# Performance work log

Measured on AMD Instinct MI355X. Metric: run time of the kernel, lower is better.

Reference implementation:

```python
import jax, jax.numpy as jnp
import numpy as np

C = 6.5  # ALCOVE specificity constant

BATCH, NE, NDIMS = 2048, 2048, 128


def setup_inputs() -> dict:
    key = jax.random.key(0)
    k1, k2, k3 = jax.random.split(key, 3)
    inputs = jax.random.normal(k1, (BATCH, NDIMS), dtype=jnp.float32)
    exemplars = jax.random.normal(k2, (NE, NDIMS), dtype=jnp.float32)
    # attn initialized to ones/ndims in the original; use positive random values
    # scaled similarly so the exp argument stays in a reasonable range.
    attn = jax.random.uniform(k3, (NDIMS,), dtype=jnp.float32) / float(NDIMS)
    return {"inputs": inputs, "exemplars": exemplars, "attn": attn}


def reference(inputs, exemplars, attn):
    # Vectorized form of: exp(-c * sum_d attn_d * |exemplars - x|) per example.
    # diff: (batch, ne, ndims)
    diff = jnp.abs(exemplars[None, :, :] - inputs[:, None, :])
    dist = jnp.einsum('bed,d->be', diff, attn)  # weighted L1 distance
    return jnp.exp(-C * dist)  # (batch, ne)
```

## Files before the change

kernel.cpp:

```cpp
#include <hip/hip_runtime.h>
#include <stdint.h>


#define BATCH 2048
#define NE 2048
#define ND 128

#define TB 64
#define TE 64
#define KC 64

#define QSCALE 16777216.0f
#define QBIAS  2097152.5f
#define KEXP   (-6.5f / 16777216.0f)

#define SAD(acc, a, b) asm("v_sad_u32 %0, %1, %2, %0" : "+v"(acc) : "v"(a), "v"(b))

__global__ __launch_bounds__(256, 4)
void alcove_rbf_kernel(const float* __restrict__ X,
                       const float* __restrict__ E,
                       const float* __restrict__ A,
                       float* __restrict__ out) {
  __shared__ uint32_t Xs[KC * TB];
  __shared__ uint32_t Es[KC * TE];

  const int tid = threadIdx.x;
  const int e0 = blockIdx.x * TE;
  const int b0 = blockIdx.y * TB;

  const int tx = tid & 15;
  const int ty = tid >> 4;
  const int lane_in = tid & 3;

  uint32_t acc[4][4];
#pragma unroll
  for (int j = 0; j < 4; ++j)
#pragma unroll
    for (int i = 0; i < 4; ++i) acc[j][i] = 0u;

  for (int kc = 0; kc < ND; kc += KC) {
    if (kc) __syncthreads();

    const float4* A4 = reinterpret_cast<const float4*>(A + kc);

#pragma unroll
    for (int it = 0; it < 4; ++it) {
      int g = it * 64 + (tid >> 2);
      int row = g & (TB - 1);
      int c4 = 4 * (g >> 6) + lane_in;
      float4 a = A4[c4];
      float4 as;
      as.x = a.x * QSCALE; as.y = a.y * QSCALE;
      as.z = a.z * QSCALE; as.w = a.w * QSCALE;
      int dbase = 4 * c4;

      float4 vx = reinterpret_cast<const float4*>(X + (size_t)(b0 + row) * ND + kc)[c4];
      Xs[(dbase + 0) * TB + row] = (uint32_t)fmaf(vx.x, as.x, QBIAS);
      Xs[(dbase + 1) * TB + row] = (uint32_t)fmaf(vx.y, as.y, QBIAS);
      Xs[(dbase + 2) * TB + row] = (uint32_t)fmaf(vx.z, as.z, QBIAS);
      Xs[(dbase + 3) * TB + row] = (uint32_t)fmaf(vx.w, as.w, QBIAS);

      float4 ve = reinterpret_cast<const float4*>(E + (size_t)(e0 + row) * ND + kc)[c4];
      Es[(dbase + 0) * TE + row] = (uint32_t)fmaf(ve.x, as.x, QBIAS);
      Es[(dbase + 1) * TE + row] = (uint32_t)fmaf(ve.y, as.y, QBIAS);
      Es[(dbase + 2) * TE + row] = (uint32_t)fmaf(ve.z, as.z, QBIAS);
      Es[(dbase + 3) * TE + row] = (uint32_t)fmaf(ve.w, as.w, QBIAS);
    }
    __syncthreads();

    const uint4* Xs4 = reinterpret_cast<const uint4*>(Xs);
    const uint4* Es4 = reinterpret_cast<const uint4*>(Es);
#pragma unroll 4
    for (int d = 0; d < KC; ++d) {
      uint4 xv = Xs4[d * (TB / 4) + ty];
      uint4 ev = Es4[d * (TE / 4) + tx];
      SAD(acc[0][0], xv.x, ev.x); SAD(acc[0][1], xv.x, ev.y);
      SAD(acc[0][2], xv.x, ev.z); SAD(acc[0][3], xv.x, ev.w);
      SAD(acc[1][0], xv.y, ev.x); SAD(acc[1][1], xv.y, ev.y);
      SAD(acc[1][2], xv.y, ev.z); SAD(acc[1][3], xv.y, ev.w);
      SAD(acc[2][0], xv.z, ev.x); SAD(acc[2][1], xv.z, ev.y);
      SAD(acc[2][2], xv.z, ev.z); SAD(acc[2][3], xv.z, ev.w);
      SAD(acc[3][0], xv.w, ev.x); SAD(acc[3][1], xv.w, ev.y);
      SAD(acc[3][2], xv.w, ev.z); SAD(acc[3][3], xv.w, ev.w);
    }
  }

#pragma unroll
  for (int j = 0; j < 4; ++j) {
    int b = b0 + 4 * ty + j;
    float4 o;
    o.x = __expf(KEXP * (float)acc[j][0]);
    o.y = __expf(KEXP * (float)acc[j][1]);
    o.z = __expf(KEXP * (float)acc[j][2]);
    o.w = __expf(KEXP * (float)acc[j][3]);
    reinterpret_cast<float4*>(out + (size_t)b * NE + e0)[tx] = o;
  }
}

extern "C" void kernel_launch(void* const* d_in, const int* in_sizes, int n_in,
                              void* d_out, int out_size, void* d_ws, size_t ws_size,
                              hipStream_t stream) {
  const float* X = (const float*)d_in[0];
  const float* E = (const float*)d_in[1];
  const float* A = (const float*)d_in[2];
  float* out = (float*)d_out;

  dim3 grid(NE / TE, BATCH / TB);
  dim3 block(256);
  alcove_rbf_kernel<<<grid, block, 0, stream>>>(X, E, A, out);
}
```

Before: 82.57 us.

## Use single-wave blocks with 8x8 register tiles and prefetched second chunk

Each block now has one 64-thread wavefront that computes the 64x64 tile with an 8x8 accumulator per thread instead of 4x4, which raises SAD work per LDS read. The LDS layout gets an XOR swizzle to avoid bank conflicts. Global loads for the second K-chunk are issued before the first chunk's compute, overlapping memory latency, and the barriers are removed because the block is a single wave. The cost is heavy VGPR use (64 accumulators plus 128 floats of prefetch) and only one wave per block, which may leave too few waves per CU to hide latency.

```diff
diff --git a/kernel.cpp b/kernel.cpp
--- a/kernel.cpp
+++ b/kernel.cpp
@@ -6,8 +6,7 @@
 #define NE 2048
 #define ND 128
 
-#define TB 64
-#define TE 64
+#define TILE 64
 #define KC 64
 
 #define QSCALE 16777216.0f
@@ -16,84 +15,119 @@
 
 #define SAD(acc, a, b) asm("v_sad_u32 %0, %1, %2, %0" : "+v"(acc) : "v"(a), "v"(b))
 
-__global__ __launch_bounds__(256, 4)
+__device__ __forceinline__ void qwrite(uint32_t* __restrict__ Xs,
+                                       uint32_t* __restrict__ Es,
+                                       const float4* fx, const float4* fe,
+                                       float4 s, int c4, int rr, int swk) {
+#pragma unroll
+  for (int t = 0; t < 16; ++t) {
+    const int wb = (4 * c4) * TILE + (((t ^ swk) << 2) + rr);
+    Xs[wb + 0 * TILE] = (uint32_t)fmaf(fx[t].x, s.x, QBIAS);
+    Xs[wb + 1 * TILE] = (uint32_t)fmaf(fx[t].y, s.y, QBIAS);
+    Xs[wb + 2 * TILE] = (uint32_t)fmaf(fx[t].z, s.z, QBIAS);
+    Xs[wb + 3 * TILE] = (uint32_t)fmaf(fx[t].w, s.w, QBIAS);
+    Es[wb + 0 * TILE] = (uint32_t)fmaf(fe[t].x, s.x, QBIAS);
+    Es[wb + 1 * TILE] = (uint32_t)fmaf(fe[t].y, s.y, QBIAS);
+    Es[wb + 2 * TILE] = (uint32_t)fmaf(fe[t].z, s.z, QBIAS);
+    Es[wb + 3 * TILE] = (uint32_t)fmaf(fe[t].w, s.w, QBIAS);
+  }
+}
+
+__device__ __forceinline__ void compute_chunk(const uint32_t* __restrict__ Xs,
+                                              const uint32_t* __restrict__ Es,
+                                              int by, int ex, uint32_t acc[8][8]) {
+  const uint4* Xs4 = (const uint4*)Xs;
+  const uint4* Es4 = (const uint4*)Es;
+#pragma unroll 2
+  for (int d4 = 0; d4 < KC; d4 += 4) {
+    const int sw = (d4 >> 2) & 7;
+    const uint4* xp = Xs4 + d4 * (TILE / 4) + (by ^ sw);
+    const uint4* ep = Es4 + d4 * (TILE / 4) + (ex ^ sw);
+#pragma unroll
+    for (int j = 0; j < 4; ++j) {
+      uint4 xa = xp[j * 16];
+      uint4 xb = xp[j * 16 + 8];
+      uint4 ea = ep[j * 16];
+      uint4 eb = ep[j * 16 + 8];
+      uint32_t xv[8] = {xa.x, xa.y, xa.z, xa.w, xb.x, xb.y, xb.z, xb.w};
+      uint32_t ev[8] = {ea.x, ea.y, ea.z, ea.w, eb.x, eb.y, eb.z, eb.w};
+#pragma unroll
+      for (int i = 0; i < 8; ++i)
+#pragma unroll
+        for (int k = 0; k < 8; ++k) SAD(acc[i][k], xv[i], ev[k]);
+    }
+  }
+}
+
+__global__ __launch_bounds__(64, 1)
 void alcove_rbf_kernel(const float* __restrict__ X,
                        const float* __restrict__ E,
                        const float* __restrict__ A,
                        float* __restrict__ out) {
-  __shared__ uint32_t Xs[KC * TB];
-  __shared__ uint32_t Es[KC * TE];
+  __shared__ uint32_t Xs[KC * TILE];
+  __shared__ uint32_t Es[KC * TILE];
 
-  const int tid = threadIdx.x;
-  const int e0 = blockIdx.x * TE;
-  const int b0 = blockIdx.y * TB;
+  const int tid = (int)threadIdx.x;
+  const int e0 = (int)blockIdx.x * TILE;
+  const int b0 = (int)blockIdx.y * TILE;
 
-  const int tx = tid & 15;
-  const int ty = tid >> 4;
-  const int lane_in = tid & 3;
+  const int ex = tid & 7;
+  const int by = tid >> 3;
+  const int c4 = tid & 15;
+  const int rr = tid >> 4;
+  const int swk = c4 & 7;
 
-  uint32_t acc[4][4];
+  uint32_t acc[8][8];
 #pragma unroll
-  for (int j = 0; j < 4; ++j)
+  for (int i = 0; i < 8; ++i)
 #pragma unroll
-    for (int i = 0; i < 4; ++i) acc[j][i] = 0u;
+    for (int k = 0; k < 8; ++k) acc[i][k] = 0u;
 
-  for (int kc = 0; kc < ND; kc += KC) {
-    if (kc) __syncthreads();
+  const float* xbase = X + (size_t)(b0 + rr) * ND + 4 * c4;
+  const float* ebase = E + (size_t)(e0 + rr) * ND + 4 * c4;
 
-    const float4* A4 = reinterpret_cast<const float4*>(A + kc);
+  float4 a0 = ((const float4*)A)[c4];
+  float4 a1 = ((const float4*)(A + KC))[c4];
+  float4 s0, s1;
+  s0.x = a0.x * QSCALE; s0.y = a0.y * QSCALE; s0.z = a0.z * QSCALE; s0.w = a0.w * QSCALE;
+  s1.x = a1.x * QSCALE; s1.y = a1.y * QSCALE; s1.z = a1.z * QSCALE; s1.w = a1.w * QSCALE;
+
+  float4 f0x[16], f0e[16];
+#pragma unroll
+  for (int t = 0; t < 16; ++t) {
+    f0x[t] = *(const float4*)(xbase + (size_t)(4 * t) * ND);
+    f0e[t] = *(const float4*)(ebase + (size_t)(4 * t) * ND);
+  }
+  qwrite(Xs, Es, f0x, f0e, s0, c4, rr, swk);
+
+  float4 f1x[16], f1e[16];
+#pragma unroll
+  for (int t = 0; t < 16; ++t) {
+    f1x[t] = *(const float4*)(xbase + (size_t)(4 * t) * ND + KC);
+    f1e[t] = *(const float4*)(ebase + (size_t)(4 * t) * ND + KC);
+  }
+
+  compute_chunk(Xs, Es, by, ex, acc);
+
+  qwrite(Xs, Es, f1x, f1e, s1, c4, rr, swk);
+
+  compute_chunk(Xs, Es, by, ex, acc);
 
 #pragma unroll
-    for (int it = 0; it < 4; ++it) {
-      int g = it * 64 + (tid >> 2);
-      int row = g & (TB - 1);
-      int c4 = 4 * (g >> 6) + lane_in;
-      float4 a = A4[c4];
-      float4 as;
-      as.x = a.x * QSCALE; as.y = a.y * QSCALE;
-      as.z = a.z * QSCALE; as.w = a.w * QSCALE;
-      int dbase = 4 * c4;
-
-      float4 vx = reinterpret_cast<const float4*>(X + (size_t)(b0 + row) * ND + kc)[c4];
-      Xs[(dbase + 0) * TB + row] = (uint32_t)fmaf(vx.x, as.x, QBIAS);
-      Xs[(dbase + 1) * TB + row] = (uint32_t)fmaf(vx.y, as.y, QBIAS);
-      Xs[(dbase + 2) * TB + row] = (uint32_t)fmaf(vx.z, as.z, QBIAS);
-      Xs[(dbase + 3) * TB + row] = (uint32_t)fmaf(vx.w, as.w, QBIAS);
-
-      float4 ve = reinterpret_cast<const float4*>(E + (size_t)(e0 + row) * ND + kc)[c4];
-      Es[(dbase + 0) * TE + row] = (uint32_t)fmaf(ve.x, as.x, QBIAS);
-      Es[(dbase + 1) * TE + row] = (uint32_t)fmaf(ve.y, as.y, QBIAS);
-      Es[(dbase + 2) * TE + row] = (uint32_t)fmaf(ve.z, as.z, QBIAS);
-      Es[(dbase + 3) * TE + row] = (uint32_t)fmaf(ve.w, as.w, QBIAS);
-    }
-    __syncthreads();
-
-    const uint4* Xs4 = reinterpret_cast<const uint4*>(Xs);
-    const uint4* Es4 = reinterpret_cast<const uint4*>(Es);
-#pragma unroll 4
-    for (int d = 0; d < KC; ++d) {
-      uint4 xv = Xs4[d * (TB / 4) + ty];
-      uint4 ev = Es4[d * (TE / 4) + tx];
-      SAD(acc[0][0], xv.x, ev.x); SAD(acc[0][1], xv.x, ev.y);
-      SAD(acc[0][2], xv.x, ev.z); SAD(acc[0][3], xv.x, ev.w);
-      SAD(acc[1][0], xv.y, ev.x); SAD(acc[1][1], xv.y, ev.y);
-      SAD(acc[1][2], xv.y, ev.z); SAD(acc[1][3], xv.y, ev.w);
-      SAD(acc[2][0], xv.z, ev.x); SAD(acc[2][1], xv.z, ev.y);
-      SAD(acc[2][2], xv.z, ev.z); SAD(acc[2][3], xv.z, ev.w);
-      SAD(acc[3][0], xv.w, ev.x); SAD(acc[3][1], xv.w, ev.y);
-      SAD(acc[3][2], xv.w, ev.z); SAD(acc[3][3], xv.w, ev.w);
-    }
-  }
-
-#pragma unroll
-  for (int j = 0; j < 4; ++j) {
-    int b = b0 + 4 * ty + j;
-    float4 o;
-    o.x = __expf(KEXP * (float)acc[j][0]);
-    o.y = __expf(KEXP * (float)acc[j][1]);
-    o.z = __expf(KEXP * (float)acc[j][2]);
-    o.w = __expf(KEXP * (float)acc[j][3]);
-    reinterpret_cast<float4*>(out + (size_t)b * NE + e0)[tx] = o;
+  for (int i = 0; i < 8; ++i) {
+    const int b = b0 + 4 * by + (i & 3) + ((i >> 2) << 5);
+    float* orow = out + (size_t)b * NE + e0;
+    float4 oA, oB;
+    oA.x = __expf(KEXP * (float)acc[i][0]);
+    oA.y = __expf(KEXP * (float)acc[i][1]);
+    oA.z = __expf(KEXP * (float)acc[i][2]);
+    oA.w = __expf(KEXP * (float)acc[i][3]);
+    oB.x = __expf(KEXP * (float)acc[i][4]);
+    oB.y = __expf(KEXP * (float)acc[i][5]);
+    oB.z = __expf(KEXP * (float)acc[i][6]);
+    oB.w = __expf(KEXP * (float)acc[i][7]);
+    *(float4*)(orow + 4 * ex) = oA;
+    *(float4*)(orow + 32 + 4 * ex) = oB;
   }
 }
 
@@ -105,7 +139,7 @@
   const float* A = (const float*)d_in[2];
   float* out = (float*)d_out;
 
-  dim3 grid(NE / TE, BATCH / TB);
-  dim3 block(256);
+  dim3 grid(NE / TILE, BATCH / TILE);
+  dim3 block(64);
   alcove_rbf_kernel<<<grid, block, 0, stream>>>(X, E, A, out);
 }
```

Result: slower. 85.77 us (+3.9%).

## Pack two 16-bit quantized dims per word and use v_sad_u16

Applied to the files above, without the earlier changes.

Quantizes attention-scaled inputs to 16-bit fixed point and packs two dimensions into each 32-bit word, so one v_sad_u16 accumulates two absolute differences. This halves the SAD instruction count and the LDS traffic, and lets all 128 dims fit in one shared tile, which removes the K-chunk loop and its extra barrier. The cost is lower quantization precision (scale 2^19 instead of 2^24), which could break accuracy tolerance, and values may clip if they fall outside the 16-bit range.

```diff
diff --git a/kernel.cpp b/kernel.cpp
--- a/kernel.cpp
+++ b/kernel.cpp
@@ -8,29 +8,30 @@
 
 #define TB 64
 #define TE 64
-#define KC 64
+#define ND2 64
 
-#define QSCALE 16777216.0f
-#define QBIAS  2097152.5f
-#define KEXP   (-6.5f / 16777216.0f)
+#define QSCALE 524288.0f
+#define QBIAS  32768.5f
+#define KEXP   (-6.5f / 524288.0f)
 
-#define SAD(acc, a, b) asm("v_sad_u32 %0, %1, %2, %0" : "+v"(acc) : "v"(a), "v"(b))
+#define SAD16(acc, a, b) asm("v_sad_u16 %0, %1, %2, %0" : "+v"(acc) : "v"(a), "v"(b))
 
 __global__ __launch_bounds__(256, 4)
 void alcove_rbf_kernel(const float* __restrict__ X,
                        const float* __restrict__ E,
                        const float* __restrict__ A,
                        float* __restrict__ out) {
-  __shared__ uint32_t Xs[KC * TB];
-  __shared__ uint32_t Es[KC * TE];
+  __shared__ uint32_t Xs[ND2 * TB];
+  __shared__ uint32_t Es[ND2 * TE];
 
-  const int tid = threadIdx.x;
-  const int e0 = blockIdx.x * TE;
-  const int b0 = blockIdx.y * TB;
+  const int tid = (int)threadIdx.x;
+  const int e0 = (int)blockIdx.x * TE;
+  const int b0 = (int)blockIdx.y * TB;
 
   const int tx = tid & 15;
   const int ty = tid >> 4;
   const int lane_in = tid & 3;
+  const int srow = tid >> 2;
 
   uint32_t acc[4][4];
 #pragma unroll
@@ -38,56 +39,51 @@
 #pragma unroll
     for (int i = 0; i < 4; ++i) acc[j][i] = 0u;
 
-  for (int kc = 0; kc < ND; kc += KC) {
-    if (kc) __syncthreads();
+  const float4* A4 = (const float4*)A;
+#pragma unroll
+  for (int it = 0; it < 8; ++it) {
+    const int c4 = 4 * it + lane_in;
+    const float4 a = A4[c4];
+    const float sx = a.x * QSCALE, sy = a.y * QSCALE,
+                sz = a.z * QSCALE, sw = a.w * QSCALE;
+    const float4 vx = *(const float4*)(X + (size_t)(b0 + srow) * ND + 4 * c4);
+    const float4 ve = *(const float4*)(E + (size_t)(e0 + srow) * ND + 4 * c4);
 
-    const float4* A4 = reinterpret_cast<const float4*>(A + kc);
+    const uint32_t x0 = ((uint32_t)fmaf(vx.x, sx, QBIAS)) |
+                        (((uint32_t)fmaf(vx.y, sy, QBIAS)) << 16);
+    const uint32_t x1 = ((uint32_t)fmaf(vx.z, sz, QBIAS)) |
+                        (((uint32_t)fmaf(vx.w, sw, QBIAS)) << 16);
+    const uint32_t e0w = ((uint32_t)fmaf(ve.x, sx, QBIAS)) |
+                         (((uint32_t)fmaf(ve.y, sy, QBIAS)) << 16);
+    const uint32_t e1w = ((uint32_t)fmaf(ve.z, sz, QBIAS)) |
+                         (((uint32_t)fmaf(ve.w, sw, QBIAS)) << 16);
 
-#pragma unroll
-    for (int it = 0; it < 4; ++it) {
-      int g = it * 64 + (tid >> 2);
-      int row = g & (TB - 1);
-      int c4 = 4 * (g >> 6) + lane_in;
-      float4 a = A4[c4];
-      float4 as;
-      as.x = a.x * QSCALE; as.y = a.y * QSCALE;
-      as.z = a.z * QSCALE; as.w = a.w * QSCALE;
-      int dbase = 4 * c4;
+    Xs[(2 * c4 + 0) * TB + srow] = x0;
+    Xs[(2 * c4 + 1) * TB + srow] = x1;
+    Es[(2 * c4 + 0) * TE + srow] = e0w;
+    Es[(2 * c4 + 1) * TE + srow] = e1w;
+  }
+  __syncthreads();
 
-      float4 vx = reinterpret_cast<const float4*>(X + (size_t)(b0 + row) * ND + kc)[c4];
-      Xs[(dbase + 0) * TB + row] = (uint32_t)fmaf(vx.x, as.x, QBIAS);
-      Xs[(dbase + 1) * TB + row] = (uint32_t)fmaf(vx.y, as.y, QBIAS);
-      Xs[(dbase + 2) * TB + row] = (uint32_t)fmaf(vx.z, as.z, QBIAS);
-      Xs[(dbase + 3) * TB + row] = (uint32_t)fmaf(vx.w, as.w, QBIAS);
-
-      float4 ve = reinterpret_cast<const float4*>(E + (size_t)(e0 + row) * ND + kc)[c4];
-      Es[(dbase + 0) * TE + row] = (uint32_t)fmaf(ve.x, as.x, QBIAS);
-      Es[(dbase + 1) * TE + row] = (uint32_t)fmaf(ve.y, as.y, QBIAS);
-      Es[(dbase + 2) * TE + row] = (uint32_t)fmaf(ve.z, as.z, QBIAS);
-      Es[(dbase + 3) * TE + row] = (uint32_t)fmaf(ve.w, as.w, QBIAS);
-    }
-    __syncthreads();
-
-    const uint4* Xs4 = reinterpret_cast<const uint4*>(Xs);
-    const uint4* Es4 = reinterpret_cast<const uint4*>(Es);
-#pragma unroll 4
-    for (int d = 0; d < KC; ++d) {
-      uint4 xv = Xs4[d * (TB / 4) + ty];
-      uint4 ev = Es4[d * (TE / 4) + tx];
-      SAD(acc[0][0], xv.x, ev.x); SAD(acc[0][1], xv.x, ev.y);
-      SAD(acc[0][2], xv.x, ev.z); SAD(acc[0][3], xv.x, ev.w);
-      SAD(acc[1][0], xv.y, ev.x); SAD(acc[1][1], xv.y, ev.y);
-      SAD(acc[1][2], xv.y, ev.z); SAD(acc[1][3], xv.y, ev.w);
-      SAD(acc[2][0], xv.z, ev.x); SAD(acc[2][1], xv.z, ev.y);
-      SAD(acc[2][2], xv.z, ev.z); SAD(acc[2][3], xv.z, ev.w);
-      SAD(acc[3][0], xv.w, ev.x); SAD(acc[3][1], xv.w, ev.y);
-      SAD(acc[3][2], xv.w, ev.z); SAD(acc[3][3], xv.w, ev.w);
-    }
+  const uint4* Xs4 = (const uint4*)Xs;
+  const uint4* Es4 = (const uint4*)Es;
+#pragma unroll 8
+  for (int d2 = 0; d2 < ND2; ++d2) {
+    const uint4 xv = Xs4[d2 * (TB / 4) + ty];
+    const uint4 ev = Es4[d2 * (TE / 4) + tx];
+    SAD16(acc[0][0], xv.x, ev.x); SAD16(acc[0][1], xv.x, ev.y);
+    SAD16(acc[0][2], xv.x, ev.z); SAD16(acc[0][3], xv.x, ev.w);
+    SAD16(acc[1][0], xv.y, ev.x); SAD16(acc[1][1], xv.y, ev.y);
+    SAD16(acc[1][2], xv.y, ev.z); SAD16(acc[1][3], xv.y, ev.w);
+    SAD16(acc[2][0], xv.z, ev.x); SAD16(acc[2][1], xv.z, ev.y);
+    SAD16(acc[2][2], xv.z, ev.z); SAD16(acc[2][3], xv.z, ev.w);
+    SAD16(acc[3][0], xv.w, ev.x); SAD16(acc[3][1], xv.w, ev.y);
+    SAD16(acc[3][2], xv.w, ev.z); SAD16(acc[3][3], xv.w, ev.w);
   }
 
 #pragma unroll
   for (int j = 0; j < 4; ++j) {
-    int b = b0 + 4 * ty + j;
+    const int b = b0 + 4 * ty + j;
     float4 o;
     o.x = __expf(KEXP * (float)acc[j][0]);
     o.y = __expf(KEXP * (float)acc[j][1]);
```

Result: faster. 73.92 us (-10.5%).
